# Performance work log

Measured on AMD Instinct MI355X. Metric: run time of the kernel, lower is better.

## Reference

```python
import jax, jax.numpy as jnp
import numpy as np

B, N, D = 4, 2048, 512
H, HD = 8, 64  # heads, output_dim per head


def setup_inputs() -> dict:
    key = jax.random.key(0)
    ks = jax.random.split(key, 6)
    x = jax.random.normal(ks[0], (B, N, D), dtype=jnp.float32)
    adj = (jax.random.uniform(ks[1], (N, N)) < 0.1).astype(jnp.float32)
    adj = jnp.maximum(adj, jnp.eye(N, dtype=jnp.float32))
    s = 0.02
    Wq = jax.random.normal(ks[2], (D, H * HD), dtype=jnp.float32) * s
    Wk = jax.random.normal(ks[3], (D, H * HD), dtype=jnp.float32) * s
    Wv = jax.random.normal(ks[4], (D, H * HD), dtype=jnp.float32) * s
    bq = jnp.zeros((H * HD,), dtype=jnp.float32)
    bk = jnp.zeros((H * HD,), dtype=jnp.float32)
    bv = jnp.zeros((H * HD,), dtype=jnp.float32)
    return {"x": x, "adj": adj, "Wq": Wq, "bq": bq, "Wk": Wk, "bk": bk, "Wv": Wv, "bv": bv}


def reference(x, adj, Wq, bq, Wk, bk, Wv, bv):
    b, n, _ = x.shape
    q = (x @ Wq + bq).reshape(b, n, H, HD)
    k = (x @ Wk + bk).reshape(b, n, H, HD)
    v = (x @ Wv + bv).reshape(b, n, H, HD)
    # scores: [b, h, i, j]
    scores = jnp.einsum('bihd,bjhd->bhij', q, k) / jnp.sqrt(jnp.float32(HD))
    mask = jnp.where(adj == 0, jnp.float32(-1e9), jnp.float32(0.0))  # [n, n]
    scores = scores + mask[None, None, :, :]
    weights = jax.nn.softmax(scores, axis=-1)
    # dropout is identity at inference (training=False)
    out = jnp.einsum('bhij,bjhd->bihd', weights, v)
    return out.reshape(b, n, H * HD)
```

## Files before the change

### kernel.cpp

```cpp
#include <hip/hip_runtime.h>
#include <hip/hip_bf16.h>
#include <stdint.h>

#define NTOK 2048
#define DIN  512
#define QSCALE 0.18033688011112042f

typedef __attribute__((ext_vector_type(8))) short bf16x8;
typedef __attribute__((ext_vector_type(4))) short bf16x4;
typedef __attribute__((ext_vector_type(4))) float f32x4;

#define MFMA16(a, b, c) __builtin_amdgcn_mfma_f32_16x16x32_bf16((a), (b), (c), 0, 0, 0)

static __device__ __forceinline__ short f2bf(float f) {
  union { float f; uint32_t u; } v; v.f = f;
  uint32_t r = (v.u + 0x7FFFu + ((v.u >> 16) & 1u)) >> 16;
  return (short)r;
}

__global__ __launch_bounds__(256) void k_xbf(const float* __restrict__ x, short* __restrict__ xb) {
  size_t i = (size_t)blockIdx.x * 256 + threadIdx.x;
  const float4 v = *(const float4*)(x + i * 4);
  bf16x4 h;
  h[0] = f2bf(v.x); h[1] = f2bf(v.y); h[2] = f2bf(v.z); h[3] = f2bf(v.w);
  *(bf16x4*)(xb + i * 4) = h;
}

__global__ __launch_bounds__(256) void k_wt(const float* __restrict__ W, short* __restrict__ Wt) {
  __shared__ float tile[32][33];
  int bo = blockIdx.x * 32, bc = blockIdx.y * 32;
  int tx = threadIdx.x & 31, ty = threadIdx.x >> 5;
#pragma unroll
  for (int q = 0; q < 4; ++q)
    tile[ty + q * 8][tx] = W[(bc + ty + q * 8) * DIN + bo + tx];
  __syncthreads();
#pragma unroll
  for (int q = 0; q < 4; ++q)
    Wt[(bo + ty + q * 8) * DIN + bc + tx] = f2bf(tile[tx][ty + q * 8]);
}

__global__ __launch_bounds__(256) void k_mask(const float* __restrict__ adj,
                                              unsigned long long* __restrict__ m64) {
  int wid = ((blockIdx.x * blockDim.x + threadIdx.x) >> 6);
  int lane = threadIdx.x & 63;
  int i = wid >> 5, wd = wid & 31;
  float a = adj[i * NTOK + wd * 64 + lane];
  unsigned long long b = __ballot(a != 0.0f);
  if (lane == 0) m64[i * 32 + wd] = b;
}

__global__ __launch_bounds__(256) void k_qkv(const short* __restrict__ xb,
                                             const short* __restrict__ Wt,
                                             const float* __restrict__ bq,
                                             const float* __restrict__ bk,
                                             const float* __restrict__ bv,
                                             short* __restrict__ Qb, short* __restrict__ Kb,
                                             short* __restrict__ Vb) {
  __shared__ short As[128 * 40];
  __shared__ short Bs[128 * 40];
  const int z = blockIdx.z;
  const short* Wz = Wt + z * DIN * DIN;
  const float* bias = (z == 0) ? bq : ((z == 1) ? bk : bv);
  const int mbase = blockIdx.x * 128, nbase = blockIdx.y * 128;
  const int tid = threadIdx.x;
  const int lane = tid & 63, w = tid >> 6;
  const int wr = w >> 1, wc = w & 1;
  const int lrow = lane & 15, lgrp = lane >> 4;

  f32x4 acc[4][4];
#pragma unroll
  for (int a = 0; a < 4; ++a)
#pragma unroll
    for (int b = 0; b < 4; ++b) acc[a][b] = (f32x4){0.f, 0.f, 0.f, 0.f};

  for (int kb = 0; kb < DIN; kb += 32) {
#pragma unroll
    for (int t = 0; t < 2; ++t) {
      int idx = tid + t * 256;
      int r = idx >> 2, c8 = idx & 3;
      *(bf16x8*)(As + r * 40 + c8 * 8) =
          *(const bf16x8*)(xb + (size_t)(mbase + r) * DIN + kb + c8 * 8);
    }
#pragma unroll
    for (int t = 0; t < 2; ++t) {
      int idx = tid + t * 256;
      int r = idx >> 2, c8 = idx & 3;
      *(bf16x8*)(Bs + r * 40 + c8 * 8) =
          *(const bf16x8*)(Wz + (size_t)(nbase + r) * DIN + kb + c8 * 8);
    }
    __syncthreads();
    bf16x8 af[4], bf[4];
#pragma unroll
    for (int mi = 0; mi < 4; ++mi)
      af[mi] = *(bf16x8*)(As + (wr * 64 + mi * 16 + lrow) * 40 + lgrp * 8);
#pragma unroll
    for (int ni = 0; ni < 4; ++ni)
      bf[ni] = *(bf16x8*)(Bs + (wc * 64 + ni * 16 + lrow) * 40 + lgrp * 8);
#pragma unroll
    for (int mi = 0; mi < 4; ++mi)
#pragma unroll
      for (int ni = 0; ni < 4; ++ni) acc[mi][ni] = MFMA16(af[mi], bf[ni], acc[mi][ni]);
    __syncthreads();
  }

#pragma unroll
  for (int ni = 0; ni < 4; ++ni) {
    int go = nbase + wc * 64 + ni * 16 + lrow;
    float bv_ = bias[go];
    int h = go >> 6, d = go & 63;
#pragma unroll
    for (int mi = 0; mi < 4; ++mi) {
#pragma unroll
      for (int v = 0; v < 4; ++v) {
        int gm = mbase + wr * 64 + mi * 16 + lgrp * 4 + v;
        int b = gm >> 11, n = gm & 2047;
        int bh = b * 8 + h;
        float val = acc[mi][ni][v] + bv_;
        if (z == 0)
          Qb[(size_t)bh * (NTOK * 64) + n * 64 + d] = f2bf(val * QSCALE);
        else if (z == 1)
          Kb[(size_t)bh * (NTOK * 64) + n * 64 + d] = f2bf(val);
        else
          Vb[(size_t)bh * (64 * NTOK) + d * NTOK + n] = f2bf(val);
      }
    }
  }
}

__global__ __launch_bounds__(256, 3) void k_attn(const short* __restrict__ Qb,
                                                 const short* __restrict__ Kb,
                                                 const short* __restrict__ Vb,
                                                 const unsigned long long* __restrict__ m64,
                                                 float* __restrict__ out) {
  __shared__ short Kl[64 * 72];
  __shared__ short Vl[64 * 72];
  __shared__ short Pl[4][32 * 72];
  const int itile = blockIdx.x, bh = blockIdx.y;
  const int ibase = itile * 128;
  const int tid = threadIdx.x, lane = tid & 63, w = tid >> 6;
  const int lrow = lane & 15, lgrp = lane >> 4;

  const short* Qp = Qb + (size_t)bh * (NTOK * 64);
  const short* Kp = Kb + (size_t)bh * (NTOK * 64);
  const short* Vp = Vb + (size_t)bh * (64 * NTOK);

  bf16x8 qa[2][2];
  const unsigned long long* mword[2];
#pragma unroll
  for (int ig = 0; ig < 2; ++ig) {
    const int qrow = ibase + ig * 64 + w * 16 + lrow;
    qa[ig][0] = *(const bf16x8*)(Qp + (size_t)qrow * 64 + lgrp * 8);
    qa[ig][1] = *(const bf16x8*)(Qp + (size_t)qrow * 64 + 32 + lgrp * 8);
    mword[ig] = m64 + (size_t)qrow * 32;
  }

  const int r0 = tid >> 3, s0 = tid & 7;

  f32x4 oacc[2][4];
#pragma unroll
  for (int ig = 0; ig < 2; ++ig)
#pragma unroll
    for (int dn = 0; dn < 4; ++dn) oacc[ig][dn] = (f32x4){0.f, 0.f, 0.f, 0.f};
  float lrun[2] = {0.f, 0.f};

  uint4 pfK0 = *(const uint4*)(Kp + (size_t)r0 * 64 + s0 * 8);
  uint4 pfK1 = *(const uint4*)(Kp + (size_t)(r0 + 32) * 64 + s0 * 8);
  uint4 pfV0 = *(const uint4*)(Vp + (size_t)r0 * NTOK + s0 * 8);
  uint4 pfV1 = *(const uint4*)(Vp + (size_t)(r0 + 32) * NTOK + s0 * 8);
  unsigned long long mw[2] = {mword[0][0], mword[1][0]};
  *(uint4*)(Kl + r0 * 72 + s0 * 8) = pfK0;
  *(uint4*)(Kl + (r0 + 32) * 72 + s0 * 8) = pfK1;
  *(uint4*)(Vl + r0 * 72 + s0 * 8) = pfV0;
  *(uint4*)(Vl + (r0 + 32) * 72 + s0 * 8) = pfV1;
  __syncthreads();

  for (int jt = 0; jt < 32; ++jt) {
    unsigned long long mwn[2] = {0ull, 0ull};
    if (jt < 31) {
      const int jn = (jt + 1) * 64;
      pfK0 = *(const uint4*)(Kp + (size_t)(jn + r0) * 64 + s0 * 8);
      pfK1 = *(const uint4*)(Kp + (size_t)(jn + r0 + 32) * 64 + s0 * 8);
      pfV0 = *(const uint4*)(Vp + (size_t)r0 * NTOK + jn + s0 * 8);
      pfV1 = *(const uint4*)(Vp + (size_t)(r0 + 32) * NTOK + jn + s0 * 8);
      mwn[0] = mword[0][jt + 1];
      mwn[1] = mword[1][jt + 1];
    }

#pragma unroll
    for (int jn = 0; jn < 4; ++jn) {
      const int krow = (jn * 16 + lrow) * 72;
      bf16x8 kf0 = *(bf16x8*)(Kl + krow + lgrp * 8);
      bf16x8 kf1 = *(bf16x8*)(Kl + krow + 32 + lgrp * 8);
#pragma unroll
      for (int ig = 0; ig < 2; ++ig) {
        f32x4 zz = (f32x4){0.f, 0.f, 0.f, 0.f};
        zz = MFMA16(kf0, qa[ig][0], zz);
        zz = MFMA16(kf1, qa[ig][1], zz);
        const uint32_t bits = (uint32_t)(mw[ig] >> (jn * 16 + lgrp * 4));
        float p0 = (bits & 1u) ? exp2f(zz[0]) : 0.f;
        float p1 = (bits & 2u) ? exp2f(zz[1]) : 0.f;
        float p2 = (bits & 4u) ? exp2f(zz[2]) : 0.f;
        float p3 = (bits & 8u) ? exp2f(zz[3]) : 0.f;
        lrun[ig] += (p0 + p1) + (p2 + p3);
        uint32_t w0, w1;
        asm("v_cvt_pk_bf16_f32 %0, %1, %2" : "=v"(w0) : "v"(p0), "v"(p1));
        asm("v_cvt_pk_bf16_f32 %0, %1, %2" : "=v"(w1) : "v"(p2), "v"(p3));
        uint2 pkv;
        pkv.x = w0;
        pkv.y = w1;
        *(uint2*)(Pl[w] + (ig * 16 + lrow) * 72 + jn * 16 + lgrp * 4) = pkv;
      }
    }

    bf16x8 pa[2][2];
#pragma unroll
    for (int ig = 0; ig < 2; ++ig)
#pragma unroll
      for (int ks = 0; ks < 2; ++ks)
        pa[ig][ks] = *(bf16x8*)(Pl[w] + (ig * 16 + lrow) * 72 + ks * 32 + lgrp * 8);
#pragma unroll
    for (int dn = 0; dn < 4; ++dn) {
#pragma unroll
      for (int ks = 0; ks < 2; ++ks) {
        bf16x8 vb = *(bf16x8*)(Vl + (dn * 16 + lrow) * 72 + ks * 32 + lgrp * 8);
#pragma unroll
        for (int ig = 0; ig < 2; ++ig) oacc[ig][dn] = MFMA16(pa[ig][ks], vb, oacc[ig][dn]);
      }
    }

    if (jt < 31) {
      __syncthreads();
      *(uint4*)(Kl + r0 * 72 + s0 * 8) = pfK0;
      *(uint4*)(Kl + (r0 + 32) * 72 + s0 * 8) = pfK1;
      *(uint4*)(Vl + r0 * 72 + s0 * 8) = pfV0;
      *(uint4*)(Vl + (r0 + 32) * 72 + s0 * 8) = pfV1;
      mw[0] = mwn[0];
      mw[1] = mwn[1];
      __syncthreads();
    }
  }

  const int b = bh >> 3, h = bh & 7;
#pragma unroll
  for (int ig = 0; ig < 2; ++ig) {
    float lfull = lrun[ig];
    lfull += __shfl_xor(lfull, 16);
    lfull += __shfl_xor(lfull, 32);
#pragma unroll
    for (int v = 0; v < 4; ++v) {
      float li = __shfl(lfull, lgrp * 4 + v);
      float inv = 1.0f / li;
      int i = ibase + ig * 64 + w * 16 + lgrp * 4 + v;
#pragma unroll
      for (int dn = 0; dn < 4; ++dn)
        out[(size_t)(b * NTOK + i) * DIN + h * 64 + dn * 16 + lrow] = oacc[ig][dn][v] * inv;
    }
  }
}

extern "C" void kernel_launch(void* const* d_in, const int* in_sizes, int n_in,
                              void* d_out, int out_size, void* d_ws, size_t ws_size,
                              hipStream_t stream) {
  const float* x   = (const float*)d_in[0];
  const float* adj = (const float*)d_in[1];
  const float* Wq  = (const float*)d_in[2];
  const float* bq  = (const float*)d_in[3];
  const float* Wk  = (const float*)d_in[4];
  const float* bk  = (const float*)d_in[5];
  const float* Wv  = (const float*)d_in[6];
  const float* bv  = (const float*)d_in[7];
  float* out = (float*)d_out;

  char* ws = (char*)d_ws;
  short* Qb = (short*)(ws);
  short* Kb = (short*)(ws + (8u << 20));
  short* Vb = (short*)(ws + (16u << 20));
  short* Wt = (short*)(ws + (24u << 20));
  unsigned long long* m64 = (unsigned long long*)(ws + (26u << 20));
  short* xb = (short*)d_out;

  k_xbf<<<4096, 256, 0, stream>>>(x, xb);
  k_wt<<<dim3(16, 16), 256, 0, stream>>>(Wq, Wt);
  k_wt<<<dim3(16, 16), 256, 0, stream>>>(Wk, Wt + 262144);
  k_wt<<<dim3(16, 16), 256, 0, stream>>>(Wv, Wt + 524288);
  k_mask<<<16384, 256, 0, stream>>>(adj, m64);
  k_qkv<<<dim3(64, 4, 3), 256, 0, stream>>>(xb, Wt, bq, bk, bv, Qb, Kb, Vb);
  k_attn<<<dim3(16, 32), 256, 0, stream>>>(Qb, Kb, Vb, m64, out);
}
```

Before: 134.4 us.

## Split attention key tile across warps and keep P in registers

The attention kernel now gives each block 64 query rows instead of 128. The four warps form a 2x2 grid: each warp covers 32 query rows and half of each 64-key tile. The probability fragments are repacked in registers to feed the PV MFMA directly, removing the per-warp LDS round trip for P. The two key-halves' partial outputs and row sums are combined through shared memory at the end. The grid doubles to 1024 blocks for better CU occupancy, at the cost of reloading each K/V tile in twice as many blocks plus an extra reduction step.

New measurement: 129.5 us. -3.7%, faster.

```diff
diff --git a/kernel.cpp b/kernel.cpp
--- a/kernel.cpp
+++ b/kernel.cpp
@@ -11,6 +11,8 @@
 typedef __attribute__((ext_vector_type(4))) float f32x4;
 
 #define MFMA16(a, b, c) __builtin_amdgcn_mfma_f32_16x16x32_bf16((a), (b), (c), 0, 0, 0)
+
+union u4bf8 { uint4 u; bf16x8 h; };
 
 static __device__ __forceinline__ short f2bf(float f) {
   union { float f; uint32_t u; } v; v.f = f;
@@ -132,12 +134,16 @@
                                                  const short* __restrict__ Vb,
                                                  const unsigned long long* __restrict__ m64,
                                                  float* __restrict__ out) {
-  __shared__ short Kl[64 * 72];
-  __shared__ short Vl[64 * 72];
-  __shared__ short Pl[4][32 * 72];
+  __shared__ char smem[18432];
+  short* Kl = (short*)smem;
+  short* Vl = (short*)(smem + 9216);
+  f32x4* ored = (f32x4*)smem;
+  float* lsum = (float*)(smem + 16384);
+
   const int itile = blockIdx.x, bh = blockIdx.y;
-  const int ibase = itile * 128;
+  const int ibase = itile * 64;
   const int tid = threadIdx.x, lane = tid & 63, w = tid >> 6;
+  const int wi = w >> 1, wj = w & 1;
   const int lrow = lane & 15, lgrp = lane >> 4;
 
   const short* Qp = Qb + (size_t)bh * (NTOK * 64);
@@ -148,7 +154,7 @@
   const unsigned long long* mword[2];
 #pragma unroll
   for (int ig = 0; ig < 2; ++ig) {
-    const int qrow = ibase + ig * 64 + w * 16 + lrow;
+    const int qrow = ibase + wi * 32 + ig * 16 + lrow;
     qa[ig][0] = *(const bf16x8*)(Qp + (size_t)qrow * 64 + lgrp * 8);
     qa[ig][1] = *(const bf16x8*)(Qp + (size_t)qrow * 64 + 32 + lgrp * 8);
     mword[ig] = m64 + (size_t)qrow * 32;
@@ -186,9 +192,10 @@
       mwn[1] = mword[1][jt + 1];
     }
 
-#pragma unroll
-    for (int jn = 0; jn < 4; ++jn) {
-      const int krow = (jn * 16 + lrow) * 72;
+    uint32_t pk[2][2][2];
+#pragma unroll
+    for (int jsub = 0; jsub < 2; ++jsub) {
+      const int krow = (wj * 32 + jsub * 16 + lrow) * 72;
       bf16x8 kf0 = *(bf16x8*)(Kl + krow + lgrp * 8);
       bf16x8 kf1 = *(bf16x8*)(Kl + krow + 32 + lgrp * 8);
 #pragma unroll
@@ -196,7 +203,7 @@
         f32x4 zz = (f32x4){0.f, 0.f, 0.f, 0.f};
         zz = MFMA16(kf0, qa[ig][0], zz);
         zz = MFMA16(kf1, qa[ig][1], zz);
-        const uint32_t bits = (uint32_t)(mw[ig] >> (jn * 16 + lgrp * 4));
+        const uint32_t bits = (uint32_t)(mw[ig] >> (wj * 32 + jsub * 16 + lgrp * 4));
         float p0 = (bits & 1u) ? exp2f(zz[0]) : 0.f;
         float p1 = (bits & 2u) ? exp2f(zz[1]) : 0.f;
         float p2 = (bits & 4u) ? exp2f(zz[2]) : 0.f;
@@ -205,26 +212,23 @@
         uint32_t w0, w1;
         asm("v_cvt_pk_bf16_f32 %0, %1, %2" : "=v"(w0) : "v"(p0), "v"(p1));
         asm("v_cvt_pk_bf16_f32 %0, %1, %2" : "=v"(w1) : "v"(p2), "v"(p3));
-        uint2 pkv;
-        pkv.x = w0;
-        pkv.y = w1;
-        *(uint2*)(Pl[w] + (ig * 16 + lrow) * 72 + jn * 16 + lgrp * 4) = pkv;
+        pk[ig][jsub][0] = w0;
+        pk[ig][jsub][1] = w1;
       }
     }
 
-    bf16x8 pa[2][2];
-#pragma unroll
-    for (int ig = 0; ig < 2; ++ig)
-#pragma unroll
-      for (int ks = 0; ks < 2; ++ks)
-        pa[ig][ks] = *(bf16x8*)(Pl[w] + (ig * 16 + lrow) * 72 + ks * 32 + lgrp * 8);
 #pragma unroll
     for (int dn = 0; dn < 4; ++dn) {
-#pragma unroll
-      for (int ks = 0; ks < 2; ++ks) {
-        bf16x8 vb = *(bf16x8*)(Vl + (dn * 16 + lrow) * 72 + ks * 32 + lgrp * 8);
-#pragma unroll
-        for (int ig = 0; ig < 2; ++ig) oacc[ig][dn] = MFMA16(pa[ig][ks], vb, oacc[ig][dn]);
+      const int vrow = (dn * 16 + lrow) * 72 + wj * 32 + lgrp * 4;
+      const uint2 v0 = *(const uint2*)(Vl + vrow);
+      const uint2 v1 = *(const uint2*)(Vl + vrow + 16);
+      u4bf8 vb;
+      vb.u = (uint4){v0.x, v0.y, v1.x, v1.y};
+#pragma unroll
+      for (int ig = 0; ig < 2; ++ig) {
+        u4bf8 pa;
+        pa.u = (uint4){pk[ig][0][0], pk[ig][0][1], pk[ig][1][0], pk[ig][1][1]};
+        oacc[ig][dn] = MFMA16(pa.h, vb.h, oacc[ig][dn]);
       }
     }
 
@@ -240,20 +244,42 @@
     }
   }
 
-  const int b = bh >> 3, h = bh & 7;
+  __syncthreads();
+
 #pragma unroll
   for (int ig = 0; ig < 2; ++ig) {
-    float lfull = lrun[ig];
-    lfull += __shfl_xor(lfull, 16);
-    lfull += __shfl_xor(lfull, 32);
-#pragma unroll
-    for (int v = 0; v < 4; ++v) {
-      float li = __shfl(lfull, lgrp * 4 + v);
-      float inv = 1.0f / li;
-      int i = ibase + ig * 64 + w * 16 + lgrp * 4 + v;
+    float s = lrun[ig];
+    s += __shfl_xor(s, 16);
+    s += __shfl_xor(s, 32);
+    if (lane < 16) lsum[(w * 2 + ig) * 16 + lane] = s;
+  }
+  if (wj == 1) {
+#pragma unroll
+    for (int ig = 0; ig < 2; ++ig)
 #pragma unroll
       for (int dn = 0; dn < 4; ++dn)
-        out[(size_t)(b * NTOK + i) * DIN + h * 64 + dn * 16 + lrow] = oacc[ig][dn][v] * inv;
+        ored[((wi * 2 + ig) * 4 + dn) * 64 + lane] = oacc[ig][dn];
+  }
+  __syncthreads();
+
+  if (wj == 0) {
+    const int b = bh >> 3, h = bh & 7;
+#pragma unroll
+    for (int ig = 0; ig < 2; ++ig) {
+      const f32x4 la = *(const f32x4*)&lsum[((wi * 2 + 0) * 2 + ig) * 16 + lgrp * 4];
+      const f32x4 lb = *(const f32x4*)&lsum[((wi * 2 + 1) * 2 + ig) * 16 + lgrp * 4];
+      float inv[4];
+#pragma unroll
+      for (int v = 0; v < 4; ++v) inv[v] = 1.0f / (la[v] + lb[v]);
+#pragma unroll
+      for (int dn = 0; dn < 4; ++dn) {
+        f32x4 s = oacc[ig][dn] + ored[((wi * 2 + ig) * 4 + dn) * 64 + lane];
+#pragma unroll
+        for (int v = 0; v < 4; ++v) {
+          int i = ibase + wi * 32 + ig * 16 + lgrp * 4 + v;
+          out[(size_t)(b * NTOK + i) * DIN + h * 64 + dn * 16 + lrow] = s[v] * inv[v];
+        }
+      }
     }
   }
 }
@@ -285,5 +311,5 @@
   k_wt<<<dim3(16, 16), 256, 0, stream>>>(Wv, Wt + 524288);
   k_mask<<<16384, 256, 0, stream>>>(adj, m64);
   k_qkv<<<dim3(64, 4, 3), 256, 0, stream>>>(xb, Wt, bq, bk, bv, Qb, Kb, Vb);
-  k_attn<<<dim3(16, 32), 256, 0, stream>>>(Qb, Kb, Vb, m64, out);
-}
+  k_attn<<<dim3(32, 32), 256, 0, stream>>>(Qb, Kb, Vb, m64, out);
+}
```
